# Kernel tuning notes

Measured on AMD Instinct MI355X. Metric: run time of the kernel, lower is better.

## Reference

```python
import jax, jax.numpy as jnp
import numpy as np
import math

B, T, D = 2, 2048, 1024
H = 16
DH = D // H  # 64
ROPE_BASE = 10000.0


def _rope_tables(seq_len, d_head, dtype=jnp.float32):
    inv_freq = 1.0 / (ROPE_BASE ** (jnp.arange(0, d_head, 2, dtype=jnp.float32) / d_head))
    pos = jnp.arange(seq_len, dtype=jnp.float32)
    freqs = jnp.outer(pos, inv_freq)            # [T, DH/2]
    emb = jnp.concatenate([freqs, freqs], -1)   # [T, DH]
    return jnp.cos(emb).astype(dtype), jnp.sin(emb).astype(dtype)


def _rotate_half(x):
    half = x.shape[-1] // 2
    return jnp.concatenate([-x[..., half:], x[..., :half]], axis=-1)


def setup_inputs() -> dict:
    key = jax.random.key(0)
    k1, k2, k3 = jax.random.split(key, 3)
    x = jax.random.normal(k1, (B, T, D), dtype=jnp.float32)
    qkv_w = jax.random.normal(k2, (D, 3 * D), dtype=jnp.float32) * (1.0 / math.sqrt(D))
    out_w = jax.random.normal(k3, (D, D), dtype=jnp.float32) * (1.0 / math.sqrt(D))
    out_b = jnp.zeros((D,), dtype=jnp.float32)
    mask = jnp.tril(jnp.ones((T, T), dtype=bool))[None, None]  # causal [1,1,T,T]
    return {"x": x, "mask": mask, "qkv_w": qkv_w, "out_w": out_w, "out_b": out_b}


def reference(x, mask, qkv_w, out_w, out_b):
    Bv, Tv, Dv = x.shape
    qkv = (x @ qkv_w).reshape(Bv, Tv, 3, H, DH)
    # [B, H, T, DH]
    q = jnp.transpose(qkv[:, :, 0], (0, 2, 1, 3))
    k = jnp.transpose(qkv[:, :, 1], (0, 2, 1, 3))
    v = jnp.transpose(qkv[:, :, 2], (0, 2, 1, 3))
    cos, sin = _rope_tables(Tv, DH, x.dtype)
    cos = cos[None, None]  # [1,1,T,DH]
    sin = sin[None, None]
    q = q * cos + _rotate_half(q) * sin
    k = k * cos + _rotate_half(k) * sin
    scores = jnp.einsum('bhqd,bhkd->bhqk', q, k) / math.sqrt(DH)
    scores = jnp.where(mask, scores, -jnp.inf)
    probs = jax.nn.softmax(scores, axis=-1)  # dropout = identity in eval mode
    out = jnp.einsum('bhqk,bhkd->bhqd', probs, v)
    out = jnp.transpose(out, (0, 2, 1, 3)).reshape(Bv, Tv, Dv)
    return out @ out_w + out_b
```

## Files before the change

kernel.cpp:

```cpp
#include <hip/hip_runtime.h>
#include <math.h>

typedef __attribute__((ext_vector_type(8))) short short8;
typedef __attribute__((ext_vector_type(4))) float f32x4;

static __device__ __forceinline__ unsigned short f2bf(float f) {
  unsigned u = __builtin_bit_cast(unsigned, f);
  u += 0x7fffu + ((u >> 16) & 1u);
  return (unsigned short)(u >> 16);
}
static __device__ __forceinline__ float bf2f(unsigned short h) {
  return __builtin_bit_cast(float, ((unsigned)h) << 16);
}
static __device__ __forceinline__ unsigned pack2bf(float a, float b) {
  return (unsigned)f2bf(a) | ((unsigned)f2bf(b) << 16);
}
static __device__ __forceinline__ unsigned pack2bf_t(float a, float b) {
  return __builtin_amdgcn_perm(__builtin_bit_cast(unsigned, b),
                               __builtin_bit_cast(unsigned, a), 0x07060302u);
}

typedef __attribute__((address_space(3))) unsigned short lds_us;
typedef __attribute__((address_space(1))) const unsigned short gbl_us;

static __device__ __forceinline__ void gld_lds16(const unsigned short* g,
                                                 unsigned short* l) {
  __builtin_amdgcn_global_load_lds((gbl_us*)g, (lds_us*)l, 16, 0, 0);
}

__global__ __launch_bounds__(256) void prep(const float* __restrict__ x,
                                            unsigned short* __restrict__ xb,
                                            const float* __restrict__ qkv_w,
                                            unsigned short* __restrict__ wqkvT,
                                            const float* __restrict__ out_w,
                                            unsigned short* __restrict__ woT) {
  __shared__ unsigned short T[64][68];
  const int blk = blockIdx.x;
  if (blk < 2048) {
    int i = (blk * 256 + threadIdx.x) * 8;
    float4 a = *(const float4*)(x + i);
    float4 b = *(const float4*)(x + i + 4);
    ushort4 u0 = {f2bf(a.x), f2bf(a.y), f2bf(a.z), f2bf(a.w)};
    ushort4 u1 = {f2bf(b.x), f2bf(b.y), f2bf(b.z), f2bf(b.w)};
    *(ushort4*)(xb + i) = u0;
    *(ushort4*)(xb + i + 4) = u1;
    return;
  }
  const float* in;
  unsigned short* out;
  int R, C, bx, by;
  if (blk < 2816) {
    in = qkv_w; out = wqkvT; R = 1024; C = 3072;
    bx = (blk - 2048) % 48; by = (blk - 2048) / 48;
  } else {
    in = out_w; out = woT; R = 1024; C = 1024;
    bx = (blk - 2816) % 16; by = (blk - 2816) / 16;
  }
  const int r0 = by * 64, c0 = bx * 64;
  const int tr = threadIdx.x >> 2;
  const int tc = (threadIdx.x & 3) * 16;
#pragma unroll
  for (int j = 0; j < 4; ++j) {
    float4 v = *(const float4*)(in + (size_t)(r0 + tr) * C + c0 + tc + j * 4);
    ushort4 u = {f2bf(v.x), f2bf(v.y), f2bf(v.z), f2bf(v.w)};
    *(ushort4*)&T[tr][tc + j * 4] = u;
  }
  __syncthreads();
  const int oc = tr;
#pragma unroll
  for (int g = 0; g < 4; ++g) {
    ushort4 u;
    u.x = T[tc + g * 4 + 0][oc];
    u.y = T[tc + g * 4 + 1][oc];
    u.z = T[tc + g * 4 + 2][oc];
    u.w = T[tc + g * 4 + 3][oc];
    *(ushort4*)(out + (size_t)(c0 + oc) * R + r0 + tc + g * 4) = u;
  }
}

__global__ __launch_bounds__(512) void gemm_qkv512(
    const unsigned short* __restrict__ A, const unsigned short* __restrict__ BT,
    unsigned short* __restrict__ qo, unsigned short* __restrict__ ko,
    unsigned short* __restrict__ vo) {
  __shared__ unsigned short As[2][4096];
  __shared__ unsigned short Bs[2][4096];
  const int tid = threadIdx.x;
  const int w = tid >> 6;
  const int lane = tid & 63;
  const int l15 = lane & 15;
  const int quad = lane >> 4;
  const int wm = w >> 2;
  const int wn = w & 3;
  const int m0 = blockIdx.y * 128;
  const int n0 = blockIdx.x * 128;

  f32x4 acc[4][2];
  const f32x4 zero4 = {0.f, 0.f, 0.f, 0.f};
#pragma unroll
  for (int mt = 0; mt < 4; ++mt)
#pragma unroll
    for (int nt = 0; nt < 2; ++nt) acc[mt][nt] = zero4;

  const int srow = tid >> 2;
  const int skch = (tid & 3) ^ ((srow >> 1) & 3);
  const int coff = tid * 8;
  const unsigned short* gA = A + (size_t)(m0 + srow) * 1024 + skch * 8;
  const unsigned short* gB = BT + (size_t)(n0 + srow) * 1024 + skch * 8;

  const int swz = (quad ^ ((l15 >> 1) & 3)) * 8;
  int aoff[4], boff[2];
#pragma unroll
  for (int t = 0; t < 4; ++t)
    aoff[t] = (wm * 64 + t * 16 + l15) * 32 + swz;
#pragma unroll
  for (int t = 0; t < 2; ++t)
    boff[t] = ((wn >> 1) * 64 + (wn & 1) * 16 + t * 32 + l15) * 32 + swz;

  auto issue = [&](int k0, int buf) {
    gld_lds16(gA + k0, &As[buf][coff]);
    gld_lds16(gB + k0, &Bs[buf][coff]);
  };

  issue(0, 0);
  for (int it = 0; it < 32; ++it) {
    const int cur = it & 1;
    __syncthreads();
    if (it + 1 < 32) issue((it + 1) * 32, cur ^ 1);

    short8 af[4], bf[2];
#pragma unroll
    for (int t = 0; t < 4; ++t) af[t] = *(const short8*)(&As[cur][aoff[t]]);
#pragma unroll
    for (int t = 0; t < 2; ++t) bf[t] = *(const short8*)(&Bs[cur][boff[t]]);
#pragma unroll
    for (int mt = 0; mt < 4; ++mt)
#pragma unroll
      for (int nt = 0; nt < 2; ++nt)
        acc[mt][nt] =
            __builtin_amdgcn_mfma_f32_16x16x32_bf16(af[mt], bf[nt], acc[mt][nt], 0, 0, 0);
  }

  const int b = m0 >> 11;
  const int ngrp = n0 + (wn >> 1) * 64;
  const int which = ngrp >> 10;
  const int h = (ngrp & 1023) >> 6;
  const int bh = b * 16 + h;
  if (which < 2) {
    unsigned short* dst = which ? ko : qo;
    const float qs = (which == 0) ? 0.1803368801111f : 1.0f;
    const int p = (wn & 1) * 16 + l15;
    float inv = __builtin_amdgcn_exp2f((float)p * -0.41524101186f) *
                0.15915494309f;
#pragma unroll
    for (int mt = 0; mt < 4; ++mt)
#pragma unroll
      for (int r = 0; r < 4; ++r) {
        int t = (m0 + wm * 64 + mt * 16 + quad * 4 + r) & 2047;
        float rv = __builtin_amdgcn_fractf((float)t * inv);
        float s = __builtin_amdgcn_sinf(rv);
        float c = __builtin_amdgcn_cosf(rv);
        float x0 = acc[mt][0][r], x1 = acc[mt][1][r];
        size_t rowoff = ((size_t)bh * 2048 + t) * 64;
        dst[rowoff + p]      = f2bf((x0 * c - x1 * s) * qs);
        dst[rowoff + p + 32] = f2bf((x1 * c + x0 * s) * qs);
      }
  } else {
#pragma unroll
    for (int mt = 0; mt < 4; ++mt) {
      int t0 = (m0 + wm * 64 + mt * 16 + quad * 4) & 2047;
#pragma unroll
      for (int nt = 0; nt < 2; ++nt) {
        int dh = (wn & 1) * 16 + nt * 32 + l15;
        ushort4 st = {f2bf(acc[mt][nt][0]), f2bf(acc[mt][nt][1]),
                      f2bf(acc[mt][nt][2]), f2bf(acc[mt][nt][3])};
        *(ushort4*)(vo + ((size_t)bh * 64 + dh) * 2048 + t0) = st;
      }
    }
  }
}

__global__ __launch_bounds__(256) void gemm_out(
    const unsigned short* __restrict__ A, const unsigned short* __restrict__ BT,
    const float* __restrict__ bias, float* __restrict__ out) {
  __shared__ unsigned short As[2][4096];
  __shared__ unsigned short Bs[2][2048];
  const int tid = threadIdx.x;
  const int w = tid >> 6;
  const int lane = tid & 63;
  const int l15 = lane & 15;
  const int quad = lane >> 4;
  const int wm = w >> 1, wn = w & 1;
  const int m0 = blockIdx.y * 128;
  const int n0 = blockIdx.x * 64;

  f32x4 acc[4][2];
  const f32x4 zero4 = {0.f, 0.f, 0.f, 0.f};
#pragma unroll
  for (int mt = 0; mt < 4; ++mt)
#pragma unroll
    for (int nt = 0; nt < 2; ++nt) acc[mt][nt] = zero4;

  int aco[2];
  const unsigned short* gA[2];
#pragma unroll
  for (int i = 0; i < 2; ++i) {
    int c = i * 256 + w * 64 + lane;
    int srow = c >> 2;
    int skch = (c & 3) ^ ((srow >> 1) & 3);
    aco[i] = c * 8;
    gA[i] = A + (size_t)(m0 + srow) * 1024 + skch * 8;
  }
  const int bc = w * 64 + lane;
  const int bsrow = bc >> 2;
  const int bskch = (bc & 3) ^ ((bsrow >> 1) & 3);
  const int bco = bc * 8;
  const unsigned short* gB = BT + (size_t)(n0 + bsrow) * 1024 + bskch * 8;

  const int swz = (quad ^ ((l15 >> 1) & 3)) * 8;
  int aoff[4], boff[2];
#pragma unroll
  for (int t = 0; t < 4; ++t) aoff[t] = (wm * 64 + t * 16 + l15) * 32 + swz;
#pragma unroll
  for (int t = 0; t < 2; ++t) boff[t] = (wn * 32 + t * 16 + l15) * 32 + swz;

  auto issue = [&](int k0, int buf) {
#pragma unroll
    for (int i = 0; i < 2; ++i) gld_lds16(gA[i] + k0, &As[buf][aco[i]]);
    gld_lds16(gB + k0, &Bs[buf][bco]);
  };

  issue(0, 0);
  for (int it = 0; it < 32; ++it) {
    const int cur = it & 1;
    __syncthreads();
    if (it + 1 < 32) issue((it + 1) * 32, cur ^ 1);

    short8 af[4], bf[2];
#pragma unroll
    for (int t = 0; t < 4; ++t) af[t] = *(const short8*)(&As[cur][aoff[t]]);
#pragma unroll
    for (int t = 0; t < 2; ++t) bf[t] = *(const short8*)(&Bs[cur][boff[t]]);
#pragma unroll
    for (int mt = 0; mt < 4; ++mt)
#pragma unroll
      for (int nt = 0; nt < 2; ++nt)
        acc[mt][nt] =
            __builtin_amdgcn_mfma_f32_16x16x32_bf16(af[mt], bf[nt], acc[mt][nt], 0, 0, 0);
  }

  const int nbase = n0 + wn * 32;
  float bv[2];
#pragma unroll
  for (int nt = 0; nt < 2; ++nt) bv[nt] = bias[nbase + nt * 16 + l15];
#pragma unroll
  for (int mt = 0; mt < 4; ++mt)
#pragma unroll
    for (int r = 0; r < 4; ++r) {
      int m = m0 + wm * 64 + mt * 16 + quad * 4 + r;
      float* orow = out + (size_t)m * 1024 + nbase + l15;
#pragma unroll
      for (int nt = 0; nt < 2; ++nt) orow[nt * 16] = acc[mt][nt][r] + bv[nt];
    }
}

__global__ __launch_bounds__(256, 7) void attn_mfma(
    const unsigned short* __restrict__ qg, const unsigned short* __restrict__ kg,
    const unsigned short* __restrict__ vtg, unsigned short* __restrict__ og,
    unsigned short* __restrict__ OpA,
    unsigned short* __restrict__ OpB,
    float* __restrict__ Lpart) {
  __shared__ unsigned short Ks[2][2048];
  __shared__ unsigned short Vt[2][2048];
  __shared__ unsigned short Ps[4 * 16 * 32];
  const int bh = blockIdx.x;
  const int slot = blockIdx.y;
  int qb, chunk;
  if (slot < 32) {
    qb = 24 + (slot & 7);
    chunk = slot >> 3;
  } else if (slot < 56) {
    int s = slot - 32;
    qb = 16 + (s & 7);
    chunk = s >> 3;
  } else if (slot < 72) {
    int s = slot - 56;
    qb = 8 + (s & 7);
    chunk = s >> 3;
  } else {
    qb = slot - 72;
    chunk = 0;
  }
  const int n = qb >= 24 ? 4 : (qb >= 16 ? 3 : (qb >= 8 ? 2 : 1));
  const int t0 = chunk * 2 * (qb + 1) / n;
  const int t1 = (chunk + 1) * 2 * (qb + 1) / n;

  const int tid = threadIdx.x;
  const int w = tid >> 6;
  const int lane = tid & 63;
  const int l15 = lane & 15;
  const int quad = lane >> 4;

  const int gq0 = qb * 64;
  const int qw = w * 16;

  const unsigned short* qrow = qg + ((size_t)bh * 2048 + gq0 + qw + l15) * 64;
  short8 qf0 = *(const short8*)(qrow + quad * 8);
  short8 qf1 = *(const short8*)(qrow + quad * 8 + 32);

  f32x4 acc_o[4];
  const f32x4 zero4 = {0.f, 0.f, 0.f, 0.f};
#pragma unroll
  for (int nt = 0; nt < 4; ++nt) acc_o[nt] = zero4;
  f32x4 acc_l = zero4;
  const short one_bf = (short)0x3F80;
  const short8 ones8 = {one_bf, one_bf, one_bf, one_bf,
                        one_bf, one_bf, one_bf, one_bf};

  const unsigned short* kbase = kg + (size_t)bh * 2048 * 64;
  const unsigned short* vtbase = vtg + (size_t)bh * 64 * 2048;
  unsigned short* pb = &Ps[w * 16 * 32];
  const int prow = l15 * 32;
  const int ksw = l15 & 7;
  const int psw = (l15 & 3) ^ ((l15 >> 2) & 3);

  const int c = w * 64 + lane;
  const int krow = c >> 3;
  const int ksc = (c & 7) ^ (krow & 7);
  const int vrow = c >> 2;
  const int vsc = ((c & 3) ^ (vrow & 3) ^ ((vrow >> 2) & 3)) & 3;
  const unsigned short* kgsrc = kbase + krow * 64 + ksc * 8;
  const unsigned short* vgsrc = vtbase + (size_t)vrow * 2048 + vsc * 8;

  auto issue = [&](int kb, int buf) {
    gld_lds16(kgsrc + kb * 32 * 64, &Ks[buf][c * 8]);
    gld_lds16(vgsrc + kb * 32, &Vt[buf][c * 8]);
  };

  const int kc0 = ((quad ^ ksw) & 7) * 8;
  const int kc1 = kc0 ^ 32;
  const int vc = ((quad ^ psw) & 3) * 8;

  issue(t0, 0);
  for (int kb = t0; kb < t1; ++kb) {
    const int cur = (kb - t0) & 1;
    __syncthreads();
    if (kb + 1 < t1) issue(kb + 1, cur ^ 1);

    const unsigned short* kt = Ks[cur];
    const unsigned short* vt = Vt[cur];

    f32x4 s[2];
#pragma unroll
    for (int nt = 0; nt < 2; ++nt) {
      const unsigned short* kr = kt + (nt * 16 + l15) * 64;
      short8 kf0 = *(const short8*)(kr + kc0);
      short8 kf1 = *(const short8*)(kr + kc1);
      f32x4 cc = zero4;
      cc = __builtin_amdgcn_mfma_f32_16x16x32_bf16(kf0, qf0, cc, 0, 0, 0);
      cc = __builtin_amdgcn_mfma_f32_16x16x32_bf16(kf1, qf1, cc, 0, 0, 0);
      s[nt] = cc;
    }

    if ((kb >> 1) == qb) {
      int gq = gq0 + qw + l15;
#pragma unroll
      for (int nt = 0; nt < 2; ++nt) {
        int gk = kb * 32 + nt * 16 + quad * 4;
#pragma unroll
        for (int r = 0; r < 4; ++r)
          if (gk + r > gq) s[nt][r] = -INFINITY;
      }
    }

#pragma unroll
    for (int nt = 0; nt < 2; ++nt) {
      float e0 = __builtin_amdgcn_exp2f(s[nt][0]);
      float e1 = __builtin_amdgcn_exp2f(s[nt][1]);
      float e2 = __builtin_amdgcn_exp2f(s[nt][2]);
      float e3 = __builtin_amdgcn_exp2f(s[nt][3]);
      int base = prow + (((nt * 2 + (quad >> 1)) ^ psw) & 3) * 8 + (quad & 1) * 4;
      uint2 pk;
      pk.x = pack2bf_t(e0, e1);
      pk.y = pack2bf_t(e2, e3);
      *(uint2*)&pb[base] = pk;
    }

    short8 pf = *(const short8*)&pb[prow + vc];

    acc_l = __builtin_amdgcn_mfma_f32_16x16x32_bf16(ones8, pf, acc_l, 0, 0, 0);

#pragma unroll
    for (int nt = 0; nt < 4; ++nt) {
      const unsigned short* vr = vt + (nt * 16 + l15) * 32;
      short8 vf = *(const short8*)(vr + vc);
      acc_o[nt] = __builtin_amdgcn_mfma_f32_16x16x32_bf16(vf, pf, acc_o[nt], 0, 0, 0);
    }
  }

  float lsum = acc_l[0];

  if (n == 1) {
    float inv_l = 1.0f / lsum;
    const int b = bh >> 4;
    const int h = bh & 15;
    unsigned short* orow =
        og + ((size_t)(b * 2048 + gq0 + qw + l15)) * 1024 + h * 64 + quad * 4;
#pragma unroll
    for (int nt = 0; nt < 4; ++nt) {
      *(unsigned*)(orow + nt * 16) =
          pack2bf(acc_o[nt][0] * inv_l, acc_o[nt][1] * inv_l);
      *(unsigned*)(orow + nt * 16 + 2) =
          pack2bf(acc_o[nt][2] * inv_l, acc_o[nt][3] * inv_l);
    }
  } else {
    const int pidx = (qb < 16) ? (qb - 8) * 2 + chunk
                               : (qb < 24) ? 16 + (qb - 16) * 3 + chunk
                                           : 40 + (qb - 24) * 4 + chunk;
    unsigned short* obase = (pidx < 16)
                                ? OpB + ((size_t)(bh * 16 + pidx)) * 4096
                                : OpA + ((size_t)(bh * 56 + (pidx - 16))) * 4096;
    unsigned short* orow = obase + (qw + l15) * 64 + quad * 4;
#pragma unroll
    for (int nt = 0; nt < 4; ++nt) {
      *(unsigned*)(orow + nt * 16) = pack2bf(acc_o[nt][0], acc_o[nt][1]);
      *(unsigned*)(orow + nt * 16 + 2) = pack2bf(acc_o[nt][2], acc_o[nt][3]);
    }
    if (quad == 0) Lpart[(bh * 72 + pidx) * 64 + qw + l15] = lsum;
  }
}

__global__ __launch_bounds__(256) void attn_combine(
    const unsigned short* __restrict__ OpA, const unsigned short* __restrict__ OpB,
    const float* __restrict__ Lpart, unsigned short* __restrict__ og) {
  int i = blockIdx.x * 256 + threadIdx.x;
  int dh = (i & 15) * 4;
  int q = (i >> 4) & 63;
  int idx = i >> 10;
  int bh = idx / 24;
  int qr = idx - bh * 24;
  int qb = 8 + qr;
  int count = qr < 8 ? 2 : (qr < 16 ? 3 : 4);
  int pstart = qr < 8 ? qr * 2 : (qr < 16 ? 16 + (qr - 8) * 3 : 40 + (qr - 16) * 4);
  float o0 = 0.f, o1 = 0.f, o2 = 0.f, o3 = 0.f, l = 0.f;
  for (int c = 0; c < count; ++c) {
    int pidx = pstart + c;
    const unsigned short* obase =
        (pidx < 16) ? OpB + ((size_t)(bh * 16 + pidx)) * 4096
                    : OpA + ((size_t)(bh * 56 + (pidx - 16))) * 4096;
    ushort4 a = *(const ushort4*)(obase + q * 64 + dh);
    o0 += bf2f(a.x);
    o1 += bf2f(a.y);
    o2 += bf2f(a.z);
    o3 += bf2f(a.w);
    l += Lpart[(bh * 72 + pidx) * 64 + q];
  }
  float inv = 1.0f / l;
  int bb = bh >> 4, h = bh & 15;
  int t = qb * 64 + q;
  unsigned short* orow = og + ((size_t)(bb * 2048 + t)) * 1024 + h * 64 + dh;
  *(unsigned*)(orow) = pack2bf(o0 * inv, o1 * inv);
  *(unsigned*)(orow + 2) = pack2bf(o2 * inv, o3 * inv);
}

extern "C" void kernel_launch(void* const* d_in, const int* in_sizes, int n_in,
                              void* d_out, int out_size, void* d_ws,
                              size_t ws_size, hipStream_t stream) {
  const float* x = (const float*)d_in[0];
  const float* qkv_w = (const float*)d_in[2];
  const float* out_w = (const float*)d_in[3];
  const float* out_b = (const float*)d_in[4];
  float* out = (float*)d_out;

  unsigned short* xb = (unsigned short*)d_ws;
  unsigned short* wqkvT = xb + 4194304;
  unsigned short* woT = wqkvT + 3145728;
  unsigned short* qb16 = woT + 1048576;
  unsigned short* kb16 = qb16 + 4194304;
  unsigned short* vt16 = kb16 + 4194304;
  unsigned short* ab = vt16 + 4194304;
  unsigned short* OpB = ab + 4194304;
  float* Lpart = (float*)(OpB + 4194304);
  unsigned short* OpA = xb;

  prep<<<3072, 256, 0, stream>>>(x, xb, qkv_w, wqkvT, out_w, woT);
  gemm_qkv512<<<dim3(24, 32), 512, 0, stream>>>(xb, wqkvT, qb16, kb16, vt16);
  attn_mfma<<<dim3(32, 80), 256, 0, stream>>>(qb16, kb16, vt16, ab, OpA, OpB,
                                              Lpart);
  attn_combine<<<3072, 256, 0, stream>>>(OpA, OpB, Lpart, ab);
  gemm_out<<<dim3(16, 32), 256, 0, stream>>>(ab, woT, out_b, out);
}
```

Measured before the change: 191.7 us.

## Use two waves per attention block, each handling 32 query rows

The attention kernel drops from four waves of 16 query rows to two waves of 32 query rows, so each K and V fragment read from LDS feeds two MFMAs instead of one. This halves LDS read traffic per unit of compute and reorganises the P buffer and the K/V load swizzle to a 64-wide row layout. In exchange each thread holds twice as many accumulators, so register pressure rises, and each block has fewer waves to hide latency.

```diff
diff --git a/kernel.cpp b/kernel.cpp
--- a/kernel.cpp
+++ b/kernel.cpp
@@ -263,7 +263,7 @@
     }
 }
 
-__global__ __launch_bounds__(256, 7) void attn_mfma(
+__global__ __launch_bounds__(128, 4) void attn_mfma(
     const unsigned short* __restrict__ qg, const unsigned short* __restrict__ kg,
     const unsigned short* __restrict__ vtg, unsigned short* __restrict__ og,
     unsigned short* __restrict__ OpA,
@@ -271,7 +271,7 @@
     float* __restrict__ Lpart) {
   __shared__ unsigned short Ks[2][2048];
   __shared__ unsigned short Vt[2][2048];
-  __shared__ unsigned short Ps[4 * 16 * 32];
+  __shared__ unsigned short Ps[2][1024];
   const int bh = blockIdx.x;
   const int slot = blockIdx.y;
   int qb, chunk;
@@ -299,46 +299,64 @@
   const int lane = tid & 63;
   const int l15 = lane & 15;
   const int quad = lane >> 4;
+  const int m7 = l15 & 7;
 
   const int gq0 = qb * 64;
-  const int qw = w * 16;
-
-  const unsigned short* qrow = qg + ((size_t)bh * 2048 + gq0 + qw + l15) * 64;
-  short8 qf0 = *(const short8*)(qrow + quad * 8);
-  short8 qf1 = *(const short8*)(qrow + quad * 8 + 32);
-
-  f32x4 acc_o[4];
+  const int qw = w * 32;
+
+  short8 qf[2][2];
+#pragma unroll
+  for (int g = 0; g < 2; ++g) {
+    const unsigned short* qrow =
+        qg + ((size_t)bh * 2048 + gq0 + qw + g * 16 + l15) * 64;
+    qf[g][0] = *(const short8*)(qrow + quad * 8);
+    qf[g][1] = *(const short8*)(qrow + quad * 8 + 32);
+  }
+
+  f32x4 acc_o[2][4];
+  f32x4 acc_l[2];
   const f32x4 zero4 = {0.f, 0.f, 0.f, 0.f};
 #pragma unroll
-  for (int nt = 0; nt < 4; ++nt) acc_o[nt] = zero4;
-  f32x4 acc_l = zero4;
+  for (int g = 0; g < 2; ++g) {
+    acc_l[g] = zero4;
+#pragma unroll
+    for (int nt = 0; nt < 4; ++nt) acc_o[g][nt] = zero4;
+  }
   const short one_bf = (short)0x3F80;
   const short8 ones8 = {one_bf, one_bf, one_bf, one_bf,
                         one_bf, one_bf, one_bf, one_bf};
 
   const unsigned short* kbase = kg + (size_t)bh * 2048 * 64;
   const unsigned short* vtbase = vtg + (size_t)bh * 64 * 2048;
-  unsigned short* pb = &Ps[w * 16 * 32];
-  const int prow = l15 * 32;
-  const int ksw = l15 & 7;
-  const int psw = (l15 & 3) ^ ((l15 >> 2) & 3);
-
-  const int c = w * 64 + lane;
-  const int krow = c >> 3;
-  const int ksc = (c & 7) ^ (krow & 7);
-  const int vrow = c >> 2;
-  const int vsc = ((c & 3) ^ (vrow & 3) ^ ((vrow >> 2) & 3)) & 3;
-  const unsigned short* kgsrc = kbase + krow * 64 + ksc * 8;
-  const unsigned short* vgsrc = vtbase + (size_t)vrow * 2048 + vsc * 8;
+  unsigned short* pb = Ps[w];
+
+  int doff[2], koff[2], voff[2];
+#pragma unroll
+  for (int i = 0; i < 2; ++i) {
+    int d = i * 128 + tid;
+    doff[i] = d * 8;
+    int r = d >> 3;
+    int lc = (d & 7) ^ (r & 7);
+    koff[i] = r * 64 + lc * 8;
+    int dh = (lc >> 2) * 32 + r;
+    voff[i] = dh * 2048 + (lc & 3) * 8;
+  }
 
   auto issue = [&](int kb, int buf) {
-    gld_lds16(kgsrc + kb * 32 * 64, &Ks[buf][c * 8]);
-    gld_lds16(vgsrc + kb * 32, &Vt[buf][c * 8]);
+#pragma unroll
+    for (int i = 0; i < 2; ++i) {
+      gld_lds16(kbase + kb * 2048 + koff[i], &Ks[buf][doff[i]]);
+      gld_lds16(vtbase + voff[i] + kb * 32, &Vt[buf][doff[i]]);
+    }
   };
 
-  const int kc0 = ((quad ^ ksw) & 7) * 8;
+  const int kc0 = ((quad ^ m7) & 7) * 8;
   const int kc1 = kc0 ^ 32;
-  const int vc = ((quad ^ psw) & 3) * 8;
+  int prd[2], vch[2];
+#pragma unroll
+  for (int g = 0; g < 2; ++g) prd[g] = l15 * 64 + (((g << 2) | quad) ^ m7) * 8;
+#pragma unroll
+  for (int h = 0; h < 2; ++h) vch[h] = (((h << 2) | quad) ^ m7) * 8;
 
   issue(t0, 0);
   for (int kb = t0; kb < t1; ++kb) {
@@ -349,68 +367,83 @@
     const unsigned short* kt = Ks[cur];
     const unsigned short* vt = Vt[cur];
 
-    f32x4 s[2];
+    f32x4 s[2][2];
 #pragma unroll
     for (int nt = 0; nt < 2; ++nt) {
       const unsigned short* kr = kt + (nt * 16 + l15) * 64;
       short8 kf0 = *(const short8*)(kr + kc0);
       short8 kf1 = *(const short8*)(kr + kc1);
-      f32x4 cc = zero4;
-      cc = __builtin_amdgcn_mfma_f32_16x16x32_bf16(kf0, qf0, cc, 0, 0, 0);
-      cc = __builtin_amdgcn_mfma_f32_16x16x32_bf16(kf1, qf1, cc, 0, 0, 0);
-      s[nt] = cc;
+#pragma unroll
+      for (int g = 0; g < 2; ++g) {
+        f32x4 cc = zero4;
+        cc = __builtin_amdgcn_mfma_f32_16x16x32_bf16(kf0, qf[g][0], cc, 0, 0, 0);
+        cc = __builtin_amdgcn_mfma_f32_16x16x32_bf16(kf1, qf[g][1], cc, 0, 0, 0);
+        s[g][nt] = cc;
+      }
     }
 
     if ((kb >> 1) == qb) {
-      int gq = gq0 + qw + l15;
+#pragma unroll
+      for (int g = 0; g < 2; ++g) {
+        int gq = gq0 + qw + g * 16 + l15;
+#pragma unroll
+        for (int nt = 0; nt < 2; ++nt) {
+          int gk = kb * 32 + nt * 16 + quad * 4;
+#pragma unroll
+          for (int r = 0; r < 4; ++r)
+            if (gk + r > gq) s[g][nt][r] = -INFINITY;
+        }
+      }
+    }
+
+#pragma unroll
+    for (int g = 0; g < 2; ++g)
 #pragma unroll
       for (int nt = 0; nt < 2; ++nt) {
-        int gk = kb * 32 + nt * 16 + quad * 4;
-#pragma unroll
-        for (int r = 0; r < 4; ++r)
-          if (gk + r > gq) s[nt][r] = -INFINITY;
-      }
-    }
-
-#pragma unroll
-    for (int nt = 0; nt < 2; ++nt) {
-      float e0 = __builtin_amdgcn_exp2f(s[nt][0]);
-      float e1 = __builtin_amdgcn_exp2f(s[nt][1]);
-      float e2 = __builtin_amdgcn_exp2f(s[nt][2]);
-      float e3 = __builtin_amdgcn_exp2f(s[nt][3]);
-      int base = prow + (((nt * 2 + (quad >> 1)) ^ psw) & 3) * 8 + (quad & 1) * 4;
-      uint2 pk;
-      pk.x = pack2bf_t(e0, e1);
-      pk.y = pack2bf_t(e2, e3);
-      *(uint2*)&pb[base] = pk;
-    }
-
-    short8 pf = *(const short8*)&pb[prow + vc];
-
-    acc_l = __builtin_amdgcn_mfma_f32_16x16x32_bf16(ones8, pf, acc_l, 0, 0, 0);
+        float e0 = __builtin_amdgcn_exp2f(s[g][nt][0]);
+        float e1 = __builtin_amdgcn_exp2f(s[g][nt][1]);
+        float e2 = __builtin_amdgcn_exp2f(s[g][nt][2]);
+        float e3 = __builtin_amdgcn_exp2f(s[g][nt][3]);
+        int cidx = ((g << 2) | (nt * 2 + (quad >> 1))) ^ m7;
+        uint2 pk;
+        pk.x = pack2bf_t(e0, e1);
+        pk.y = pack2bf_t(e2, e3);
+        *(uint2*)&pb[l15 * 64 + cidx * 8 + (quad & 1) * 4] = pk;
+      }
+
+    short8 pfa = *(const short8*)&pb[prd[0]];
+    short8 pfb = *(const short8*)&pb[prd[1]];
+
+    acc_l[0] = __builtin_amdgcn_mfma_f32_16x16x32_bf16(ones8, pfa, acc_l[0], 0, 0, 0);
+    acc_l[1] = __builtin_amdgcn_mfma_f32_16x16x32_bf16(ones8, pfb, acc_l[1], 0, 0, 0);
 
 #pragma unroll
     for (int nt = 0; nt < 4; ++nt) {
-      const unsigned short* vr = vt + (nt * 16 + l15) * 32;
-      short8 vf = *(const short8*)(vr + vc);
-      acc_o[nt] = __builtin_amdgcn_mfma_f32_16x16x32_bf16(vf, pf, acc_o[nt], 0, 0, 0);
-    }
-  }
-
-  float lsum = acc_l[0];
+      const unsigned short* vr = vt + ((nt & 1) * 16 + l15) * 64 + vch[nt >> 1];
+      short8 vf = *(const short8*)vr;
+      acc_o[0][nt] = __builtin_amdgcn_mfma_f32_16x16x32_bf16(vf, pfa, acc_o[0][nt], 0, 0, 0);
+      acc_o[1][nt] = __builtin_amdgcn_mfma_f32_16x16x32_bf16(vf, pfb, acc_o[1][nt], 0, 0, 0);
+    }
+  }
+
+  float lsum[2] = {acc_l[0][0], acc_l[1][0]};
 
   if (n == 1) {
-    float inv_l = 1.0f / lsum;
     const int b = bh >> 4;
     const int h = bh & 15;
-    unsigned short* orow =
-        og + ((size_t)(b * 2048 + gq0 + qw + l15)) * 1024 + h * 64 + quad * 4;
-#pragma unroll
-    for (int nt = 0; nt < 4; ++nt) {
-      *(unsigned*)(orow + nt * 16) =
-          pack2bf(acc_o[nt][0] * inv_l, acc_o[nt][1] * inv_l);
-      *(unsigned*)(orow + nt * 16 + 2) =
-          pack2bf(acc_o[nt][2] * inv_l, acc_o[nt][3] * inv_l);
+#pragma unroll
+    for (int g = 0; g < 2; ++g) {
+      float inv_l = 1.0f / lsum[g];
+      unsigned short* orow =
+          og + ((size_t)(b * 2048 + gq0 + qw + g * 16 + l15)) * 1024 + h * 64 +
+          quad * 4;
+#pragma unroll
+      for (int nt = 0; nt < 4; ++nt) {
+        *(unsigned*)(orow + nt * 16) =
+            pack2bf(acc_o[g][nt][0] * inv_l, acc_o[g][nt][1] * inv_l);
+        *(unsigned*)(orow + nt * 16 + 2) =
+            pack2bf(acc_o[g][nt][2] * inv_l, acc_o[g][nt][3] * inv_l);
+      }
     }
   } else {
     const int pidx = (qb < 16) ? (qb - 8) * 2 + chunk
@@ -419,13 +452,17 @@
     unsigned short* obase = (pidx < 16)
                                 ? OpB + ((size_t)(bh * 16 + pidx)) * 4096
                                 : OpA + ((size_t)(bh * 56 + (pidx - 16))) * 4096;
-    unsigned short* orow = obase + (qw + l15) * 64 + quad * 4;
-#pragma unroll
-    for (int nt = 0; nt < 4; ++nt) {
-      *(unsigned*)(orow + nt * 16) = pack2bf(acc_o[nt][0], acc_o[nt][1]);
-      *(unsigned*)(orow + nt * 16 + 2) = pack2bf(acc_o[nt][2], acc_o[nt][3]);
-    }
-    if (quad == 0) Lpart[(bh * 72 + pidx) * 64 + qw + l15] = lsum;
+#pragma unroll
+    for (int g = 0; g < 2; ++g) {
+      unsigned short* orow = obase + (qw + g * 16 + l15) * 64 + quad * 4;
+#pragma unroll
+      for (int nt = 0; nt < 4; ++nt) {
+        *(unsigned*)(orow + nt * 16) = pack2bf(acc_o[g][nt][0], acc_o[g][nt][1]);
+        *(unsigned*)(orow + nt * 16 + 2) = pack2bf(acc_o[g][nt][2], acc_o[g][nt][3]);
+      }
+      if (quad == 0)
+        Lpart[(bh * 72 + pidx) * 64 + qw + g * 16 + l15] = lsum[g];
+    }
   }
 }
 
@@ -484,7 +521,7 @@
 
   prep<<<3072, 256, 0, stream>>>(x, xb, qkv_w, wqkvT, out_w, woT);
   gemm_qkv512<<<dim3(24, 32), 512, 0, stream>>>(xb, wqkvT, qb16, kb16, vt16);
-  attn_mfma<<<dim3(32, 80), 256, 0, stream>>>(qb16, kb16, vt16, ab, OpA, OpB,
+  attn_mfma<<<dim3(32, 80), 128, 0, stream>>>(qb16, kb16, vt16, ab, OpA, OpB,
                                               Lpart);
   attn_combine<<<3072, 256, 0, stream>>>(OpA, OpB, Lpart, ab);
   gemm_out<<<dim3(16, 32), 256, 0, stream>>>(ab, woT, out_b, out);
```

Result: no change. 190.4 us (-0.7%).
